# Kernel optimization log

Hardware: AMD Instinct MI355X
Metric: run time of the kernel (lower is better)

## Reference

```python
import jax, jax.numpy as jnp
import numpy as np

PAD_WORD = 1  # index of PAD in tgt_dict


def setup_inputs() -> dict:
    key = jax.random.key(0)
    k1, k2, k3, k4, k5 = jax.random.split(key, 5)
    N, D, S = 1024, 1024, 64   # N = tlen*batch rows, D = input_size, S = slen
    B, V = 64, 32000           # batch, vocab
    hidden = jax.random.normal(k1, (N, D), dtype=jnp.float32)
    attn = jax.random.uniform(k2, (N, S), dtype=jnp.float32)
    src = jax.random.randint(k3, (S, B, 1), 0, V)
    W = jax.random.normal(k4, (V, D), dtype=jnp.float32) * 0.02
    w_copy = jax.random.normal(k5, (D, 1), dtype=jnp.float32) * 0.02
    b_copy = jnp.zeros((1,), dtype=jnp.float32)
    return {"hidden": hidden, "attn": attn, "src": src, "W": W,
            "w_copy": w_copy, "b_copy": b_copy}


def reference(hidden, attn, src, W, w_copy, b_copy):
    V = W.shape[0]
    B = src.shape[1]
    T = hidden.shape[0] // B  # tlen
    # copy gate: sigmoid(Linear(hidden, 1))  -> [N, 1]
    p_copy = jax.nn.sigmoid(hidden @ w_copy + b_copy)
    # tied-embedding projection -> [N, V], pad column masked to -inf
    logits = hidden @ W.T
    logits = logits.at[:, PAD_WORD].set(-jnp.inf)
    prob = jax.nn.softmax(logits, axis=1) + 1e-20
    # gated generation prob, reshaped to [T, B*V]
    prob = ((1.0 - p_copy) * prob).reshape(T, B * V)
    # flattened source indices with per-batch vocab offsets -> [B*S]
    batch_offset = (jnp.arange(B) * V)[:, None]
    idx = (src[:, :, 0].T + batch_offset).reshape(-1)
    # gated copy attention, reshaped to [T, B*S]
    attn_w = (p_copy * attn).reshape(T, -1)
    # scatter-add copy mass into the vocab distribution (duplicates accumulate)
    out = prob.at[:, idx].add(attn_w)
    return out.reshape(T * B, V)
```

## Files before the change

kernel.cpp:

```cpp
#include <hip/hip_runtime.h>
#include <stdint.h>

typedef unsigned char  u8;
typedef unsigned short u16;
typedef unsigned int u32;

#define NROWS 1024
#define DDIM  1024
#define SLEN  64
#define BATCH 64
#define VOCAB 32000
#define NBN2  125
#define PAD_WORD 1

typedef __attribute__((ext_vector_type(4))) float f32x4;

__device__ __forceinline__ u16 f2bf(float x) {
  union { float f; u32 u; } v; v.f = x;
  u32 r = v.u + 0x7FFF + ((v.u >> 16) & 1);
  return (u16)(r >> 16);
}
__device__ __forceinline__ float bf2f(u16 x) {
  union { u32 u; float f; } v; v.u = ((u32)x) << 16;
  return v.f;
}
__device__ __forceinline__ u32 f2e4m3(float x) {
  union { float f; u32 u; } v; v.f = x;
  const u32 s = (v.u >> 31) << 7;
  const u32 m = v.u & 0x7FFFFFFFu;
  if (m < 0x3C800000u) {
    union { u32 u; float f; } a; a.u = m;
    int q = (int)rintf(a.f * 512.0f);
    return s | (u32)q;
  }
  u32 u2 = m + 0x7FFFFu + ((m >> 20) & 1);
  u32 code = (((u2 >> 23) - 120u) << 3) | ((u2 >> 20) & 7u);
  if (code > 0x7Eu) code = 0x7Eu;
  return s | code;
}

__global__ __launch_bounds__(256) void prep_kernel(
    const float* __restrict__ hidden, const float* __restrict__ w_copy,
    const float* __restrict__ b_copy, u8* __restrict__ hq,
    float* __restrict__ pcopy)
{
  const int n = blockIdx.x;
  const int tid = threadIdx.x;
  float4 h = ((const float4*)(hidden + (size_t)n * DDIM))[tid];
  float4 w = ((const float4*)w_copy)[tid];
  u32 q = f2e4m3(h.x) | (f2e4m3(h.y) << 8) | (f2e4m3(h.z) << 16) | (f2e4m3(h.w) << 24);
  ((u32*)(hq + (size_t)n * DDIM))[tid] = q;
  float d = h.x * w.x + h.y * w.y + h.z * w.z + h.w * w.w;
  #pragma unroll
  for (int m = 1; m < 64; m <<= 1) d += __shfl_xor(d, m);
  __shared__ float ws4[4];
  if ((tid & 63) == 0) ws4[tid >> 6] = d;
  __syncthreads();
  if (tid == 0) {
    float s = ws4[0] + ws4[1] + ws4[2] + ws4[3] + b_copy[0];
    pcopy[n] = 1.0f / (1.0f + __expf(-s));
  }
}

__global__ __launch_bounds__(256) void convw8_kernel(
    const float* __restrict__ W, u8* __restrict__ Wq)
{
  const int total = VOCAB * DDIM / 16;
  const int stride = gridDim.x * blockDim.x;
  for (int i = blockIdx.x * 256 + threadIdx.x; i < total; i += stride) {
    const f32x4* p = (const f32x4*)(W + (size_t)i * 16);
    f32x4 a = p[0], b = p[1], c = p[2], d = p[3];
    uint4 q;
    q.x = f2e4m3(a.x) | (f2e4m3(a.y) << 8) | (f2e4m3(a.z) << 16) | (f2e4m3(a.w) << 24);
    q.y = f2e4m3(b.x) | (f2e4m3(b.y) << 8) | (f2e4m3(b.z) << 16) | (f2e4m3(b.w) << 24);
    q.z = f2e4m3(c.x) | (f2e4m3(c.y) << 8) | (f2e4m3(c.z) << 16) | (f2e4m3(c.w) << 24);
    q.w = f2e4m3(d.x) | (f2e4m3(d.y) << 8) | (f2e4m3(d.z) << 16) | (f2e4m3(d.w) << 24);
    ((uint4*)Wq)[i] = q;
  }
}

__global__ __launch_bounds__(512, 2) void gemm_exp_kernel(
    const u8* __restrict__ A, const u8* __restrict__ B,
    float* __restrict__ out, u16* __restrict__ ebf,
    float* __restrict__ partial, const int use_bf16)
{
  __shared__ u8 lA[2][16384];
  __shared__ u8 lB[2][16384];
  __shared__ float rowacc[4][256];

  const int tid  = threadIdx.x;
  const int lane = tid & 63;
  const int wid  = tid >> 6;
  const int wm   = wid >> 2;
  const int wn   = wid & 3;
  const int al   = lane & 15;
  const int ks   = lane >> 4;

  const int orig = blockIdx.x;
  const int xcd  = orig & 7;
  const int idx  = orig >> 3;
  const int wg   = (xcd < 4 ? xcd * 63 : 252 + (xcd - 4) * 62) + idx;
  const int bm   = wg & 3;
  const int bn   = wg >> 2;

  const u8* Abase = A + (size_t)(bm * 256) * DDIM;
  const u8* Bbase = B + (size_t)(bn * 256) * DDIM;

  const int sA = wid * 64 + lane;
  const int rA = sA >> 2;
  const int cA = (lane & 3) ^ (rA & 3);

#define GLL(gp, lp) __builtin_amdgcn_global_load_lds( \
    (const __attribute__((address_space(1))) u32*)(gp), \
    (__attribute__((address_space(3))) u32*)(lp), 16, 0, 0)
#define STAGE_T(gbase, lptr, kt) do { \
    GLL((gbase) + (size_t)rA * DDIM + (kt) + cA * 16, (lptr) + sA * 16); \
    GLL((gbase) + (size_t)(rA + 128) * DDIM + (kt) + cA * 16, (lptr) + 8192 + sA * 16); \
  } while (0)

#define WL(n) do { asm volatile("s_waitcnt lgkmcnt(" #n ")" ::: "memory"); \
                   __builtin_amdgcn_sched_barrier(0); } while (0)
#define WV(n) do { asm volatile("s_waitcnt vmcnt(" #n ")" ::: "memory"); \
                   __builtin_amdgcn_sched_barrier(0); } while (0)
#define BAR() do { __builtin_amdgcn_sched_barrier(0); \
                   __builtin_amdgcn_s_barrier(); \
                   __builtin_amdgcn_sched_barrier(0); } while (0)

#define RD_ALO(buf) do { \
    _Pragma("unroll") \
    for (int mi = 0; mi < 4; ++mi) { \
      const int r_ = wm * 128 + mi * 16 + al; \
      const u8* p_ = (buf) + r_ * 64 + (ks & 1) * 8; \
      alo[mi][0] = *(const long*)(p_ + ((((ks >> 1))     ^ (r_ & 3)) * 16)); \
      alo[mi][1] = *(const long*)(p_ + ((((ks >> 1) + 2) ^ (r_ & 3)) * 16)); \
    } } while (0)
#define RD_AHI(buf) do { \
    _Pragma("unroll") \
    for (int mi = 0; mi < 4; ++mi) { \
      const int r_ = wm * 128 + 64 + mi * 16 + al; \
      const u8* p_ = (buf) + r_ * 64 + (ks & 1) * 8; \
      ahi[mi][0] = *(const long*)(p_ + ((((ks >> 1))     ^ (r_ & 3)) * 16)); \
      ahi[mi][1] = *(const long*)(p_ + ((((ks >> 1) + 2) ^ (r_ & 3)) * 16)); \
    } } while (0)
#define RD_B0(buf) do { \
    _Pragma("unroll") \
    for (int ni = 0; ni < 2; ++ni) { \
      const int r_ = wn * 64 + ni * 16 + al; \
      const u8* p_ = (buf) + r_ * 64 + (ks & 1) * 8; \
      b0f[ni][0] = *(const long*)(p_ + ((((ks >> 1))     ^ (r_ & 3)) * 16)); \
      b0f[ni][1] = *(const long*)(p_ + ((((ks >> 1) + 2) ^ (r_ & 3)) * 16)); \
    } } while (0)
#define RD_B1(buf) do { \
    _Pragma("unroll") \
    for (int ni = 0; ni < 2; ++ni) { \
      const int r_ = wn * 64 + 32 + ni * 16 + al; \
      const u8* p_ = (buf) + r_ * 64 + (ks & 1) * 8; \
      b1f[ni][0] = *(const long*)(p_ + ((((ks >> 1))     ^ (r_ & 3)) * 16)); \
      b1f[ni][1] = *(const long*)(p_ + ((((ks >> 1) + 2) ^ (r_ & 3)) * 16)); \
    } } while (0)
#define MM(AF, BF, r0, c0) do { \
    __builtin_amdgcn_s_setprio(1); \
    _Pragma("unroll") \
    for (int mi = 0; mi < 4; ++mi) \
      _Pragma("unroll") \
      for (int ni = 0; ni < 2; ++ni) \
        _Pragma("unroll") \
        for (int kk = 0; kk < 2; ++kk) \
          acc[(r0) + mi][(c0) + ni] = __builtin_amdgcn_mfma_f32_16x16x32_fp8_fp8( \
              AF[mi][kk], BF[ni][kk], acc[(r0) + mi][(c0) + ni], 0, 0, 0); \
    __builtin_amdgcn_s_setprio(0); \
  } while (0)

  u8* lAc = &lA[0][0]; u8* lBc = &lB[0][0];
  u8* lAn = &lA[1][0]; u8* lBn = &lB[1][0];

  f32x4 acc[8][4];
  #pragma unroll
  for (int i = 0; i < 8; ++i)
    #pragma unroll
    for (int j = 0; j < 4; ++j)
      acc[i][j] = (f32x4){0.f, 0.f, 0.f, 0.f};

  long alo[4][2], ahi[4][2], b0f[2][2], b1f[2][2];

  STAGE_T(Abase, lAc, 0);
  STAGE_T(Bbase, lBc, 0);
  STAGE_T(Abase, lAn, 64);
  WV(2);
  BAR();
  RD_ALO(lAc); RD_B0(lBc); RD_B1(lBc);

  for (int t = 0; t < 15; ++t) {
    const int kt1 = (t + 1) * 64;
    const int kt2 = (t + 2) * 64;
    WL(4);
    MM(alo, b0f, 0, 0);
    STAGE_T(Bbase, lBn, kt1);
    RD_AHI(lAc);
    WL(8);
    MM(alo, b1f, 0, 2);
    WL(0);
    MM(ahi, b0f, 4, 0);
    BAR();
    if (t < 14) STAGE_T(Abase, lAc, kt2);
    if (t < 14) { WV(2); } else { WV(0); }
    BAR();
    RD_ALO(lAn); RD_B0(lBn);
    MM(ahi, b1f, 4, 2);
    RD_B1(lBn);
    u8* tp = lAc; lAc = lAn; lAn = tp;
    tp = lBc; lBc = lBn; lBn = tp;
  }
  WL(4);
  MM(alo, b0f, 0, 0);
  RD_AHI(lAc);
  WL(8);
  MM(alo, b1f, 0, 2);
  WL(0);
  MM(ahi, b0f, 4, 0);
  MM(ahi, b1f, 4, 2);

#undef GLL
#undef STAGE_T
#undef WL
#undef WV
#undef BAR

  const int g = ks;
  float rsum[8][4];
  #pragma unroll
  for (int mi = 0; mi < 8; ++mi)
    #pragma unroll
    for (int j = 0; j < 4; ++j) rsum[mi][j] = 0.f;

  const size_t grow0 = (size_t)(bm * 256 + wm * 128);
  const int gcol0 = bn * 256 + wn * 64;
  #pragma unroll
  for (int mi = 0; mi < 8; ++mi) {
    const int rofs = (mi >> 2) * 64 + (mi & 3) * 16 + g * 4;
    #pragma unroll
    for (int j = 0; j < 4; ++j) {
      const size_t row = grow0 + rofs + j;
      #pragma unroll
      for (int ni = 0; ni < 4; ++ni) {
        const int col = gcol0 + (ni >> 1) * 32 + (ni & 1) * 16 + al;
        float e = __expf(acc[mi][ni][j]);
        if (col == PAD_WORD) e = 0.f;
        rsum[mi][j] += e;
        if (use_bf16) ebf[row * VOCAB + col] = f2bf(e);
        else          out[row * VOCAB + col] = e;
      }
    }
  }
  #pragma unroll
  for (int mi = 0; mi < 8; ++mi)
    #pragma unroll
    for (int j = 0; j < 4; ++j) {
      float v = rsum[mi][j];
      v += __shfl_xor(v, 1);
      v += __shfl_xor(v, 2);
      v += __shfl_xor(v, 4);
      v += __shfl_xor(v, 8);
      rsum[mi][j] = v;
    }
  if (al == 0) {
    #pragma unroll
    for (int mi = 0; mi < 8; ++mi)
      #pragma unroll
      for (int j = 0; j < 4; ++j)
        rowacc[wn][wm * 128 + (mi >> 2) * 64 + (mi & 3) * 16 + g * 4 + j] =
            rsum[mi][j];
  }
  __syncthreads();
  if (tid < 256)
    partial[(size_t)bn * NROWS + bm * 256 + tid] =
        rowacc[0][tid] + rowacc[1][tid] + rowacc[2][tid] + rowacc[3][tid];
}

__global__ __launch_bounds__(256) void rowsum_kernel(
    const float* __restrict__ partial, const float* __restrict__ pcopy,
    float* __restrict__ scale, float* __restrict__ ofs)
{
  const int n = blockIdx.x * 256 + threadIdx.x;
  if (n >= NROWS) return;
  float s = 0.f;
  for (int j = 0; j < NBN2; ++j) s += partial[(size_t)j * NROWS + n];
  const float p = pcopy[n];
  scale[n] = (1.0f - p) / s;
  ofs[n]   = (1.0f - p) * 1e-20f;
}

__global__ __launch_bounds__(256) void norm_bf16_kernel(
    const u16* __restrict__ ebf, float* __restrict__ out,
    const float* __restrict__ scale, const float* __restrict__ ofs)
{
  const int total8 = NROWS * VOCAB / 8;
  const int stride = gridDim.x * blockDim.x;
  for (int i = blockIdx.x * 256 + threadIdx.x; i < total8; i += stride) {
    const int n = i / (VOCAB / 8);
    ushort4 v0 = ((const ushort4*)ebf)[i * 2];
    ushort4 v1 = ((const ushort4*)ebf)[i * 2 + 1];
    const float sc = scale[n], of = ofs[n];
    float4 o0, o1;
    o0.x = bf2f(v0.x) * sc + of; o0.y = bf2f(v0.y) * sc + of;
    o0.z = bf2f(v0.z) * sc + of; o0.w = bf2f(v0.w) * sc + of;
    o1.x = bf2f(v1.x) * sc + of; o1.y = bf2f(v1.y) * sc + of;
    o1.z = bf2f(v1.z) * sc + of; o1.w = bf2f(v1.w) * sc + of;
    ((float4*)out)[i * 2]     = o0;
    ((float4*)out)[i * 2 + 1] = o1;
  }
}

__global__ __launch_bounds__(256) void norm_kernel(
    float* __restrict__ out, const float* __restrict__ scale,
    const float* __restrict__ ofs)
{
  const int total4 = NROWS * VOCAB / 4;
  const int stride = gridDim.x * blockDim.x;
  for (int i = blockIdx.x * 256 + threadIdx.x; i < total4; i += stride) {
    const int n = i / (VOCAB / 4);
    float4* p = (float4*)out + i;
    float4 v = *p;
    const float sc = scale[n], of = ofs[n];
    v.x = v.x * sc + of;
    v.y = v.y * sc + of;
    v.z = v.z * sc + of;
    v.w = v.w * sc + of;
    *p = v;
  }
}

__global__ __launch_bounds__(256) void scatter_kernel(
    float* __restrict__ out, const float* __restrict__ attn,
    const int* __restrict__ src, const float* __restrict__ pcopy)
{
  const int t = blockIdx.x * 256 + threadIdx.x;
  const int n = t >> 6;
  const int s = t & 63;
  const int b = n & (BATCH - 1);
  const int v = src[s * BATCH + b];
  const float w = pcopy[n] * attn[(size_t)n * SLEN + s];
  atomicAdd(out + (size_t)n * VOCAB + v, w);
}

extern "C" void kernel_launch(void* const* d_in, const int* in_sizes, int n_in,
                              void* d_out, int out_size, void* d_ws, size_t ws_size,
                              hipStream_t stream) {
  const float* hidden = (const float*)d_in[0];
  const float* attn   = (const float*)d_in[1];
  const int*   src    = (const int*)d_in[2];
  const float* W      = (const float*)d_in[3];
  const float* w_copy = (const float*)d_in[4];
  const float* b_copy = (const float*)d_in[5];
  float* out = (float*)d_out;

  char* ws = (char*)d_ws;
  u8*    Wq      = (u8*)ws;
  u8*    hq      = (u8*)(ws + 32768000);
  float* pcopy   = (float*)(ws + 33816576);
  float* partial = (float*)(ws + 33820672);
  float* scale   = (float*)(ws + 34844672);
  float* ofs     = (float*)(ws + 34848768);
  u16*   ebf     = (u16*)(ws + 34852864);
  const size_t need_bf16 = 34852864ull + 65536000ull;
  const int use_bf16 = (ws_size >= need_bf16) ? 1 : 0;

  prep_kernel<<<NROWS, 256, 0, stream>>>(hidden, w_copy, b_copy, hq, pcopy);
  convw8_kernel<<<2048, 256, 0, stream>>>(W, Wq);
  gemm_exp_kernel<<<4 * NBN2, 512, 0, stream>>>(hq, Wq, out, ebf, partial, use_bf16);
  rowsum_kernel<<<(NROWS + 255) / 256, 256, 0, stream>>>(partial, pcopy, scale, ofs);
  if (use_bf16)
    norm_bf16_kernel<<<2048, 256, 0, stream>>>(ebf, out, scale, ofs);
  else
    norm_kernel<<<2048, 256, 0, stream>>>(out, scale, ofs);
  scatter_kernel<<<NROWS * SLEN / 256, 256, 0, stream>>>(out, attn, src, pcopy);
}
```

Before: 171.1 us.

## Pre-permute FP8 operand layout so GEMM fragments load with single 16-byte LDS reads

```diff
diff --git a/kernel.cpp b/kernel.cpp
--- a/kernel.cpp
+++ b/kernel.cpp
@@ -14,6 +14,7 @@
 #define PAD_WORD 1
 
 typedef __attribute__((ext_vector_type(4))) float f32x4;
+typedef __attribute__((ext_vector_type(2))) long i64x2;
 
 __device__ __forceinline__ u16 f2bf(float x) {
   union { float f; u32 u; } v; v.f = x;
@@ -38,6 +39,10 @@
   if (code > 0x7Eu) code = 0x7Eu;
   return s | code;
 }
+__device__ __forceinline__ u32 pk4e4m3(float4 f) {
+  return f2e4m3(f.x) | (f2e4m3(f.y) << 8) | (f2e4m3(f.z) << 16) | (f2e4m3(f.w) << 24);
+}
+
 
 __global__ __launch_bounds__(256) void prep_kernel(
     const float* __restrict__ hidden, const float* __restrict__ w_copy,
@@ -48,8 +53,12 @@
   const int tid = threadIdx.x;
   float4 h = ((const float4*)(hidden + (size_t)n * DDIM))[tid];
   float4 w = ((const float4*)w_copy)[tid];
-  u32 q = f2e4m3(h.x) | (f2e4m3(h.y) << 8) | (f2e4m3(h.z) << 16) | (f2e4m3(h.w) << 24);
-  ((u32*)(hq + (size_t)n * DDIM))[tid] = q;
+  const int kb   = tid * 4;
+  const int blk  = kb >> 6;
+  const int kk   = (kb >> 5) & 1;
+  const int u    = (kb >> 3) & 3;
+  const int off  = kb & 7;
+  ((u32*)(hq + (size_t)n * DDIM + blk * 64 + u * 16 + kk * 8 + off))[0] = pk4e4m3(h);
   float d = h.x * w.x + h.y * w.y + h.z * w.z + h.w * w.w;
   #pragma unroll
   for (int m = 1; m < 64; m <<= 1) d += __shfl_xor(d, m);
@@ -65,17 +74,21 @@
 __global__ __launch_bounds__(256) void convw8_kernel(
     const float* __restrict__ W, u8* __restrict__ Wq)
 {
-  const int total = VOCAB * DDIM / 16;
-  const int stride = gridDim.x * blockDim.x;
-  for (int i = blockIdx.x * 256 + threadIdx.x; i < total; i += stride) {
-    const f32x4* p = (const f32x4*)(W + (size_t)i * 16);
-    f32x4 a = p[0], b = p[1], c = p[2], d = p[3];
-    uint4 q;
-    q.x = f2e4m3(a.x) | (f2e4m3(a.y) << 8) | (f2e4m3(a.z) << 16) | (f2e4m3(a.w) << 24);
-    q.y = f2e4m3(b.x) | (f2e4m3(b.y) << 8) | (f2e4m3(b.z) << 16) | (f2e4m3(b.w) << 24);
-    q.z = f2e4m3(c.x) | (f2e4m3(c.y) << 8) | (f2e4m3(c.z) << 16) | (f2e4m3(c.w) << 24);
-    q.w = f2e4m3(d.x) | (f2e4m3(d.y) << 8) | (f2e4m3(d.z) << 16) | (f2e4m3(d.w) << 24);
-    ((uint4*)Wq)[i] = q;
+  const int i = blockIdx.x * 256 + threadIdx.x;
+  if (i >= VOCAB * DDIM / 64) return;
+  const float4* p = (const float4*)(W + (size_t)i * 64);
+  float4 f[16];
+  #pragma unroll
+  for (int j = 0; j < 16; ++j) f[j] = p[j];
+  uint4* q = (uint4*)(Wq + (size_t)i * 64);
+  #pragma unroll
+  for (int u = 0; u < 4; ++u) {
+    uint4 o;
+    o.x = pk4e4m3(f[2 * u]);
+    o.y = pk4e4m3(f[2 * u + 1]);
+    o.z = pk4e4m3(f[8 + 2 * u]);
+    o.w = pk4e4m3(f[8 + 2 * u + 1]);
+    q[u] = o;
   }
 }
 
@@ -108,7 +121,7 @@
 
   const int sA = wid * 64 + lane;
   const int rA = sA >> 2;
-  const int cA = (lane & 3) ^ (rA & 3);
+  const int cA = (lane & 3) ^ ((rA >> 1) & 3);
 
 #define GLL(gp, lp) __builtin_amdgcn_global_load_lds( \
     (const __attribute__((address_space(1))) u32*)(gp), \
@@ -126,38 +139,14 @@
                    __builtin_amdgcn_s_barrier(); \
                    __builtin_amdgcn_sched_barrier(0); } while (0)
 
-#define RD_ALO(buf) do { \
+#define RD_FR(dst, buf, rbase, cnt) do { \
     _Pragma("unroll") \
-    for (int mi = 0; mi < 4; ++mi) { \
-      const int r_ = wm * 128 + mi * 16 + al; \
-      const u8* p_ = (buf) + r_ * 64 + (ks & 1) * 8; \
-      alo[mi][0] = *(const long*)(p_ + ((((ks >> 1))     ^ (r_ & 3)) * 16)); \
-      alo[mi][1] = *(const long*)(p_ + ((((ks >> 1) + 2) ^ (r_ & 3)) * 16)); \
+    for (int i_ = 0; i_ < (cnt); ++i_) { \
+      const int r_ = (rbase) + i_ * 16 + al; \
+      i64x2 v_ = *(const i64x2*)((buf) + r_ * 64 + (ks ^ ((r_ >> 1) & 3)) * 16); \
+      dst[i_][0] = v_.x; dst[i_][1] = v_.y; \
     } } while (0)
-#define RD_AHI(buf) do { \
-    _Pragma("unroll") \
-    for (int mi = 0; mi < 4; ++mi) { \
-      const int r_ = wm * 128 + 64 + mi * 16 + al; \
-      const u8* p_ = (buf) + r_ * 64 + (ks & 1) * 8; \
-      ahi[mi][0] = *(const long*)(p_ + ((((ks >> 1))     ^ (r_ & 3)) * 16)); \
-      ahi[mi][1] = *(const long*)(p_ + ((((ks >> 1) + 2) ^ (r_ & 3)) * 16)); \
-    } } while (0)
-#define RD_B0(buf) do { \
-    _Pragma("unroll") \
-    for (int ni = 0; ni < 2; ++ni) { \
-      const int r_ = wn * 64 + ni * 16 + al; \
-      const u8* p_ = (buf) + r_ * 64 + (ks & 1) * 8; \
-      b0f[ni][0] = *(const long*)(p_ + ((((ks >> 1))     ^ (r_ & 3)) * 16)); \
-      b0f[ni][1] = *(const long*)(p_ + ((((ks >> 1) + 2) ^ (r_ & 3)) * 16)); \
-    } } while (0)
-#define RD_B1(buf) do { \
-    _Pragma("unroll") \
-    for (int ni = 0; ni < 2; ++ni) { \
-      const int r_ = wn * 64 + 32 + ni * 16 + al; \
-      const u8* p_ = (buf) + r_ * 64 + (ks & 1) * 8; \
-      b1f[ni][0] = *(const long*)(p_ + ((((ks >> 1))     ^ (r_ & 3)) * 16)); \
-      b1f[ni][1] = *(const long*)(p_ + ((((ks >> 1) + 2) ^ (r_ & 3)) * 16)); \
-    } } while (0)
+
 #define MM(AF, BF, r0, c0) do { \
     __builtin_amdgcn_s_setprio(1); \
     _Pragma("unroll") \
@@ -188,16 +177,18 @@
   STAGE_T(Abase, lAn, 64);
   WV(2);
   BAR();
-  RD_ALO(lAc); RD_B0(lBc); RD_B1(lBc);
+  RD_FR(alo, lAc, wm * 128, 4);
+  RD_FR(b0f, lBc, wn * 64, 2);
+  RD_FR(b1f, lBc, wn * 64 + 32, 2);
 
   for (int t = 0; t < 15; ++t) {
     const int kt1 = (t + 1) * 64;
     const int kt2 = (t + 2) * 64;
-    WL(4);
+    WL(2);
     MM(alo, b0f, 0, 0);
     STAGE_T(Bbase, lBn, kt1);
-    RD_AHI(lAc);
-    WL(8);
+    RD_FR(ahi, lAc, wm * 128 + 64, 4);
+    WL(4);
     MM(alo, b1f, 0, 2);
     WL(0);
     MM(ahi, b0f, 4, 0);
@@ -205,16 +196,17 @@
     if (t < 14) STAGE_T(Abase, lAc, kt2);
     if (t < 14) { WV(2); } else { WV(0); }
     BAR();
-    RD_ALO(lAn); RD_B0(lBn);
+    RD_FR(alo, lAn, wm * 128, 4);
+    RD_FR(b0f, lBn, wn * 64, 2);
     MM(ahi, b1f, 4, 2);
-    RD_B1(lBn);
+    RD_FR(b1f, lBn, wn * 64 + 32, 2);
     u8* tp = lAc; lAc = lAn; lAn = tp;
     tp = lBc; lBc = lBn; lBn = tp;
   }
+  WL(2);
+  MM(alo, b0f, 0, 0);
+  RD_FR(ahi, lAc, wm * 128 + 64, 4);
   WL(4);
-  MM(alo, b0f, 0, 0);
-  RD_AHI(lAc);
-  WL(8);
   MM(alo, b1f, 0, 2);
   WL(0);
   MM(ahi, b0f, 4, 0);
@@ -225,6 +217,7 @@
 #undef WL
 #undef WV
 #undef BAR
+#undef RD_FR
 
   const int g = ks;
   float rsum[8][4];
@@ -366,7 +359,7 @@
   const int use_bf16 = (ws_size >= need_bf16) ? 1 : 0;
 
   prep_kernel<<<NROWS, 256, 0, stream>>>(hidden, w_copy, b_copy, hq, pcopy);
-  convw8_kernel<<<2048, 256, 0, stream>>>(W, Wq);
+  convw8_kernel<<<VOCAB * DDIM / 64 / 256, 256, 0, stream>>>(W, Wq);
   gemm_exp_kernel<<<4 * NBN2, 512, 0, stream>>>(hq, Wq, out, ebf, partial, use_bf16);
   rowsum_kernel<<<(NROWS + 255) / 256, 256, 0, stream>>>(partial, pcopy, scale, ofs);
   if (use_bf16)
```

After: 160.0 us. -6.5%, faster.
